# Optimization experiments

Hardware: AMD Instinct MI355X
Metric: run time of the kernel (lower is better)

Reference implementation:

```python
import jax, jax.numpy as jnp
import numpy as np

V, H, I, L = 32000, 1024, 2048, 4
NH, NKV, HD = 16, 8, 64
E, K = 4, 2
B, S = 2, 1024
NEG = jnp.finfo(jnp.float32).min


def setup_inputs() -> dict:
    key = jax.random.key(0)
    ks = jax.random.split(key, 11)
    w = lambda k, shape: jax.random.normal(k, shape, jnp.float32) * 0.02
    return dict(
        input_ids=jax.random.randint(ks[0], (B, S), 0, V),
        embed=w(ks[1], (V, H)),
        Wq=w(ks[2], (L, H, NH * HD)),
        Wk=w(ks[3], (L, H, NKV * HD)),
        Wv=w(ks[4], (L, H, NKV * HD)),
        Wo=w(ks[5], (L, NH * HD, H)),
        ln1=jnp.ones((L, H), jnp.float32),
        ln2=jnp.ones((L, H), jnp.float32),
        gate=w(ks[6], (L, H, E)),
        Wg=w(ks[7], (L, E, H, I)),
        Wu=w(ks[8], (L, E, H, I)),
        Wd=w(ks[9], (L, E, I, H)),
        norm_w=jnp.ones((H,), jnp.float32),
        lm_head=w(ks[10], (H, V)),
    )


def rmsnorm(x, w, eps=1e-6):
    var = jnp.mean(x * x, axis=-1, keepdims=True)
    return w * (x * jax.lax.rsqrt(var + eps))


def forward(input_ids, embed, Wq, Wk, Wv, Wo, ln1, ln2, gate, Wg, Wu, Wd, norm_w, lm_head):
    b, s = input_ids.shape
    h = embed[input_ids]  # [B,S,H]
    mask = jnp.where(jnp.triu(jnp.ones((s, s), bool), 1), NEG, 0.0)[None, None]  # causal [1,1,S,S]
    inv_sqrt_hd = 1.0 / np.sqrt(HD)
    rep = NH // NKV

    def step(h, p):
        wq, wk, wv, wo, l1, l2, gw, wg, wu, wd = p
        x = rmsnorm(h, l1)
        q = (x @ wq).reshape(b, s, NH, HD).transpose(0, 2, 1, 3)    # [B,NH,S,HD]
        k = (x @ wk).reshape(b, s, NKV, HD).transpose(0, 2, 1, 3)   # [B,NKV,S,HD]
        v = (x @ wv).reshape(b, s, NKV, HD).transpose(0, 2, 1, 3)
        k = jnp.repeat(k, rep, axis=1)  # GQA repeat_kv
        v = jnp.repeat(v, rep, axis=1)
        scores = jnp.einsum('bhqd,bhkd->bhqk', q, k) * inv_sqrt_hd + mask
        attn = jax.nn.softmax(scores, axis=-1)
        o = jnp.einsum('bhqk,bhkd->bhqd', attn, v).transpose(0, 2, 1, 3).reshape(b, s, NH * HD)
        h = h + o @ wo
        # MoE FFN (top-k routing, combine via per-expert gate weights)
        x = rmsnorm(h, l2).reshape(b * s, H)              # [T,H]
        probs = jax.nn.softmax(x @ gw, axis=-1)           # [T,E]
        topk_p, topk_i = jax.lax.top_k(probs, K)          # [T,K]
        comb = jnp.sum(topk_p[..., None] * jax.nn.one_hot(topk_i, E, dtype=x.dtype), axis=1)  # [T,E]
        g = jax.nn.silu(jnp.einsum('th,ehi->eti', x, wg))  # [E,T,I]
        u = jnp.einsum('th,ehi->eti', x, wu)
        eo = jnp.einsum('eti,eih->eth', g * u, wd)         # [E,T,H]
        moe = jnp.einsum('eth,te->th', eo, comb).reshape(b, s, H)
        return h + moe, None

    h, _ = jax.lax.scan(step, h, (Wq, Wk, Wv, Wo, ln1, ln2, gate, Wg, Wu, Wd))
    return rmsnorm(h, norm_w) @ lm_head  # [B,S,V]


def reference(input_ids, embed, Wq, Wk, Wv, Wo, ln1, ln2, gate, Wg, Wu, Wd, norm_w, lm_head):
    return forward(input_ids, embed, Wq, Wk, Wv, Wo, ln1, ln2, gate, Wg, Wu, Wd, norm_w, lm_head)
```

## Files before the change

kernel.cpp:

```cpp
#include <hip/hip_runtime.h>

#define T_ 2048
#define H_ 1024
#define S_ 1024
#define V_ 32000
#define I_ 2048
#define NHD 1024
#define KVD 512

typedef unsigned short u16;
typedef unsigned int u32;
typedef __attribute__((ext_vector_type(8))) short s16x8;
typedef __attribute__((ext_vector_type(4))) float f32x4;

__device__ __forceinline__ u16 f2b(float f){ u32 x=__builtin_bit_cast(u32,f); return (u16)((x+0x7fffu+((x>>16)&1u))>>16); }
__device__ __forceinline__ float b2f(u16 u){ return __builtin_bit_cast(float,(u32)u<<16); }
__device__ __forceinline__ float wsum(float v){ for(int o=32;o;o>>=1) v+=__shfl_xor(v,o); return v; }

__device__ __forceinline__ void gl16(const void* g, void* l){
  __builtin_amdgcn_global_load_lds(
      (const __attribute__((address_space(1))) unsigned int*)g,
      (__attribute__((address_space(3))) unsigned int*)l, 16, 0, 0);
}

__global__ void k_embed(const int* __restrict__ ids, const float* __restrict__ emb,
                        float* __restrict__ h, int* __restrict__ cnt){
  if(blockIdx.x==0 && threadIdx.x<16) cnt[threadIdx.x]=0;
  int t = blockIdx.x;
  long src = (long)ids[t]*H_;
  ((float4*)(h + (long)t*H_))[threadIdx.x] = ((const float4*)(emb+src))[threadIdx.x];
}

__global__ void k_rms_sp(const float* __restrict__ h, const float* __restrict__ w,
                         u16* __restrict__ xhi, u16* __restrict__ xlo){
  int wid = threadIdx.x>>6, lane = threadIdx.x&63;
  int t = blockIdx.x*4 + wid;
  const float* row = h + (long)t*H_;
  float v[16]; float ss=0.f;
  #pragma unroll
  for(int j=0;j<16;j++){ v[j]=row[j*64+lane]; ss += v[j]*v[j]; }
  ss = wsum(ss);
  float rstd = rsqrtf(ss/(float)H_ + 1e-6f);
  #pragma unroll
  for(int j=0;j<16;j++){
    int idx=j*64+lane;
    float y = v[j]*rstd*w[idx];
    u16 hv = f2b(y);
    xhi[(long)t*H_+idx] = hv;
    if(xlo) xlo[(long)t*H_+idx] = f2b(y - b2f(hv));
  }
}

__global__ void k_router(const float* __restrict__ h, const float* __restrict__ lw,
                         const float* __restrict__ gate, float* __restrict__ comb,
                         int* __restrict__ lists, int* __restrict__ cnt, int2* __restrict__ epos,
                         u16* __restrict__ xhi, u16* __restrict__ xlo){
  int wid = threadIdx.x>>6, lane = threadIdx.x&63;
  int t = blockIdx.x*4+wid;
  const float* row = h + (long)t*H_;
  float v[16]; float ss=0.f;
  #pragma unroll
  for(int j=0;j<16;j++){ v[j]=row[j*64+lane]; ss+=v[j]*v[j]; }
  ss = wsum(ss);
  float rstd = rsqrtf(ss/(float)H_+1e-6f);
  float a0=0,a1=0,a2=0,a3=0;
  #pragma unroll
  for(int j=0;j<16;j++){
    int idx=j*64+lane;
    float y = v[j]*rstd*lw[idx];
    u16 hv = f2b(y);
    xhi[(long)t*H_+idx] = hv;
    xlo[(long)t*H_+idx] = f2b(y - b2f(hv));
    float4 g4 = ((const float4*)gate)[idx];
    a0 += y*g4.x; a1 += y*g4.y; a2 += y*g4.z; a3 += y*g4.w;
  }
  a0=wsum(a0); a1=wsum(a1); a2=wsum(a2); a3=wsum(a3);
  if(lane==0){
    float p[4]={a0,a1,a2,a3};
    float m = fmaxf(fmaxf(p[0],p[1]),fmaxf(p[2],p[3]));
    float s=0; for(int e=0;e<4;e++){ p[e]=__expf(p[e]-m); s+=p[e]; }
    for(int e=0;e<4;e++) p[e]/=s;
    int i1=0; for(int e=1;e<4;e++) if(p[e]>p[i1]) i1=e;
    int i2=-1; for(int e=0;e<4;e++){ if(e==i1) continue; if(i2<0||p[e]>p[i2]) i2=e; }
    float* c = comb + (long)t*4;
    for(int e=0;e<4;e++) c[e] = (e==i1||e==i2)? p[e] : 0.f;
    int p1 = atomicAdd(&cnt[i1],1); lists[i1*T_+p1]=t;
    int p2 = atomicAdd(&cnt[i2],1); lists[i2*T_+p2]=t;
    epos[t] = make_int2((p1<<2)|i1, (p2<<2)|i2);
  }
}

__global__ void k_transpose(const float* __restrict__ in, u16* __restrict__ hi, u16* __restrict__ lo,
                            int R, int C, long zi, long zo){
  __shared__ float tile[32][33];
  in += (long)blockIdx.z*zi; hi += (long)blockIdx.z*zo; if(lo) lo += (long)blockIdx.z*zo;
  int c0 = blockIdx.x*32, r0 = blockIdx.y*32;
  int tx = threadIdx.x, ty = threadIdx.y;
  #pragma unroll
  for(int i=0;i<4;i++) tile[ty+8*i][tx] = in[(long)(r0+ty+8*i)*C + c0+tx];
  __syncthreads();
  #pragma unroll
  for(int i=0;i<4;i++){
    int cc=ty+8*i; float v = tile[tx][cc];
    u16 hv = f2b(v);
    long idx = (long)(c0+cc)*R + r0+tx;
    hi[idx] = hv;
    if(lo) lo[idx] = f2b(v - b2f(hv));
  }
}

__global__ void k_wtrans(const float* __restrict__ Wq, const float* __restrict__ Wk,
                         const float* __restrict__ Wv, const float* __restrict__ Wo,
                         const float* __restrict__ Wg, const float* __restrict__ Wu,
                         const float* __restrict__ Wd,
                         u16* __restrict__ qkvh, u16* __restrict__ qkvl,
                         u16* __restrict__ oh, u16* __restrict__ ol,
                         u16* __restrict__ gh, u16* __restrict__ gl_,
                         u16* __restrict__ uh, u16* __restrict__ ul,
                         u16* __restrict__ dh, u16* __restrict__ dl)
{
  __shared__ float tile[32][33];
  int id = blockIdx.x;
  const float* in; u16 *hi, *lo; int R, C, bx, by;
  if(id < 1024){ in=Wq; hi=qkvh; lo=qkvl; R=1024; C=1024; bx=id&31; by=id>>5; }
  else if(id < 1536){ id-=1024; in=Wk; hi=qkvh+1048576; lo=qkvl+1048576; R=1024; C=512; bx=id&15; by=id>>4; }
  else if(id < 2048){ id-=1536; in=Wv; hi=qkvh+1572864; lo=qkvl+1572864; R=1024; C=512; bx=id&15; by=id>>4; }
  else if(id < 3072){ id-=2048; in=Wo; hi=oh; lo=ol; R=1024; C=1024; bx=id&31; by=id>>5; }
  else if(id < 11264){ id-=3072; int z=id>>11, r2=id&2047;
    in=Wg+(size_t)z*H_*I_; hi=gh+(size_t)z*I_*H_; lo=gl_+(size_t)z*I_*H_;
    R=1024; C=2048; bx=r2&63; by=r2>>6; }
  else if(id < 19456){ id-=11264; int z=id>>11, r2=id&2047;
    in=Wu+(size_t)z*H_*I_; hi=uh+(size_t)z*I_*H_; lo=ul+(size_t)z*I_*H_;
    R=1024; C=2048; bx=r2&63; by=r2>>6; }
  else { id-=19456; int z=id>>11, r2=id&2047;
    in=Wd+(size_t)z*I_*H_; hi=dh+(size_t)z*H_*I_; lo=dl+(size_t)z*H_*I_;
    R=2048; C=1024; bx=r2&31; by=r2>>5; }
  int c0=bx*32, r0=by*32, tx=threadIdx.x, ty=threadIdx.y;
  #pragma unroll
  for(int i=0;i<4;i++) tile[ty+8*i][tx] = in[(long)(r0+ty+8*i)*C + c0+tx];
  __syncthreads();
  #pragma unroll
  for(int i=0;i<4;i++){
    int cc=ty+8*i; float v = tile[tx][cc];
    u16 hv = f2b(v);
    long idx = (long)(c0+cc)*R + r0+tx;
    hi[idx] = hv;
    lo[idx] = f2b(v - b2f(hv));
  }
}

__global__ void k_combine(float* __restrict__ h, const float* __restrict__ eo,
                          const int2* __restrict__ epos, const float* __restrict__ comb,
                          const float* __restrict__ wn, u16* __restrict__ xhi, u16* __restrict__ xlo){
  int t = blockIdx.x, c = threadIdx.x;
  int lane = c&63, wid = c>>6;
  int2 ep = epos[t];
  int e1 = ep.x&3, p1 = ep.x>>2, e2 = ep.y&3, p2 = ep.y>>2;
  float c1 = comb[t*4+e1], c2 = comb[t*4+e2];
  float4 a = ((const float4*)(eo + (long)(e1*T_+p1)*H_))[c];
  float4 b = ((const float4*)(eo + (long)(e2*T_+p2)*H_))[c];
  float4* hp = (float4*)(h + (long)t*H_) + c;
  float4 hv = *hp;
  hv.x += c1*a.x + c2*b.x; hv.y += c1*a.y + c2*b.y;
  hv.z += c1*a.z + c2*b.z; hv.w += c1*a.w + c2*b.w;
  *hp = hv;
  __shared__ float red[4];
  float ss = hv.x*hv.x + hv.y*hv.y + hv.z*hv.z + hv.w*hv.w;
  ss = wsum(ss);
  if(lane==0) red[wid]=ss;
  __syncthreads();
  float tot = red[0]+red[1]+red[2]+red[3];
  float rstd = rsqrtf(tot*(1.f/1024.f) + 1e-6f);
  float4 wv = ((const float4*)wn)[c];
  float y0=hv.x*rstd*wv.x, y1=hv.y*rstd*wv.y, y2=hv.z*rstd*wv.z, y3=hv.w*rstd*wv.w;
  ushort4 Hv; Hv.x=f2b(y0); Hv.y=f2b(y1); Hv.z=f2b(y2); Hv.w=f2b(y3);
  ((ushort4*)(xhi + (long)t*H_))[c] = Hv;
  if(xlo){
    ushort4 Lv;
    Lv.x=f2b(y0-b2f(Hv.x)); Lv.y=f2b(y1-b2f(Hv.y));
    Lv.z=f2b(y2-b2f(Hv.z)); Lv.w=f2b(y3-b2f(Hv.w));
    ((ushort4*)(xlo + (long)t*H_))[c] = Lv;
  }
}

__global__ __launch_bounds__(512) void k_flash(
  const u16* __restrict__ qh_g, const u16* __restrict__ ql_g,
  const u16* __restrict__ kh_g, const u16* __restrict__ kl_g,
  const u16* __restrict__ vth_g, const u16* __restrict__ vtl_g,
  u16* __restrict__ oh_g, u16* __restrict__ ol_g)
{
  __shared__ alignas(16) u16 Kh[8192], Kl[8192];
  __shared__ alignas(16) u16 Vh[8192], Vl[8192];
  __shared__ alignas(16) u16 Ph[16384], Pl[16384];
  const int qt = blockIdx.x, hh = blockIdx.y, b = blockIdx.z;
  const int hk = hh>>1;
  const int lane = threadIdx.x&63, w = threadIdx.x>>6;
  const int rA = lane&15, kg = (lane>>4)*8;

  s16x8 qfh[2], qfl[2];
  {
    long t = (long)(b*1024+qt*128) + w*16 + rA;
    const u16* qp = qh_g + t*NHD + hh*64;
    const u16* qp2= ql_g + t*NHD + hh*64;
    qfh[0]=*(const s16x8*)(qp + kg);      qfh[1]=*(const s16x8*)(qp + 32 + kg);
    qfl[0]=*(const s16x8*)(qp2 + kg);     qfl[1]=*(const s16x8*)(qp2 + 32 + kg);
  }

  const int ktend = qt+1;
  {
    const u16* kp = kh_g + ((long)(b*1024))*KVD + hk*64;
    const u16* kp2= kl_g + ((long)(b*1024))*KVD + hk*64;
    #pragma unroll
    for(int s=0;s<2;s++){
      int idx=s*8+w, hf=idx>>3, g=idx&7;
      int row = g*16 + (lane>>2);
      int c8  = hf*32 + (lane&3)*8;
      gl16(kp  + (long)row*KVD + c8, &Kh[hf*4096 + g*512]);
      gl16(kp2 + (long)row*KVD + c8, &Kl[hf*4096 + g*512]);
    }
  }

  f32x4 Oa[4];
  float mrun[4], lrun[4];
  #pragma unroll
  for(int jn=0;jn<4;jn++){ f32x4 zv={0.f,0.f,0.f,0.f}; Oa[jn]=zv; }
  #pragma unroll
  for(int r=0;r<4;r++){ mrun[r]=-3.0e38f; lrun[r]=0.f; }

  __syncthreads();

  for(int kt=0; kt<ktend; kt++){
    {
      const u16* vp = vth_g + (long)b*((long)KVD*S_) + (long)(hk*64)*S_ + kt*128;
      const u16* vp2= vtl_g + (long)b*((long)KVD*S_) + (long)(hk*64)*S_ + kt*128;
      #pragma unroll
      for(int s=0;s<2;s++){
        int idx=s*8+w, ks=idx>>2, g=idx&3;
        int dr = g*16 + (lane>>2);
        int k8 = (lane&3)*8;
        gl16(vp  + (long)dr*S_ + ks*32 + k8, &Vh[ks*2048 + g*512]);
        gl16(vp2 + (long)dr*S_ + ks*32 + k8, &Vl[ks*2048 + g*512]);
      }
    }

    f32x4 Sf[8];
    #pragma unroll
    for(int j=0;j<8;j++){ f32x4 zv={0.f,0.f,0.f,0.f}; Sf[j]=zv; }
    #pragma unroll
    for(int k2=0;k2<2;k2++){
      s16x8 bh[8],bl[8];
      #pragma unroll
      for(int j=0;j<8;j++){
        int ky = j*16+rA;
        bh[j]=*(const s16x8*)&Kh[k2*4096 + ky*32 + kg];
        bl[j]=*(const s16x8*)&Kl[k2*4096 + ky*32 + kg];
      }
      #pragma unroll
      for(int j=0;j<8;j++){
        Sf[j]=__builtin_amdgcn_mfma_f32_16x16x32_bf16(qfh[k2],bh[j],Sf[j],0,0,0);
        Sf[j]=__builtin_amdgcn_mfma_f32_16x16x32_bf16(qfh[k2],bl[j],Sf[j],0,0,0);
        Sf[j]=__builtin_amdgcn_mfma_f32_16x16x32_bf16(qfl[k2],bh[j],Sf[j],0,0,0);
      }
    }

    const bool last = (kt==ktend-1);
    #pragma unroll
    for(int j=0;j<8;j++)
      #pragma unroll
      for(int r=0;r<4;r++){
        float sv = Sf[j][r]*0.125f;
        if(last){
          int qr = qt*128 + w*16 + ((lane>>4)<<2) + r;
          int ky = kt*128 + j*16 + (lane&15);
          if(ky>qr) sv = -3.0e38f;
        }
        Sf[j][r]=sv;
      }

    float mt[4];
    #pragma unroll
    for(int r=0;r<4;r++){
      float v = Sf[0][r];
      #pragma unroll
      for(int j=1;j<8;j++) v = fmaxf(v, Sf[j][r]);
      v=fmaxf(v,__shfl_xor(v,1)); v=fmaxf(v,__shfl_xor(v,2));
      v=fmaxf(v,__shfl_xor(v,4)); v=fmaxf(v,__shfl_xor(v,8));
      mt[r]=v;
    }

    #pragma unroll
    for(int r=0;r<4;r++){
      float mo=mrun[r];
      float mn=fmaxf(mo,mt[r]);
      float al_=__expf(mo-mn);
      mrun[r]=mn;
      lrun[r]*=al_;
      #pragma unroll
      for(int jn=0;jn<4;jn++) Oa[jn][r]*=al_;
    }

    float ls[4];
    #pragma unroll
    for(int r=0;r<4;r++) ls[r]=0.f;
    #pragma unroll
    for(int j=0;j<8;j++)
      #pragma unroll
      for(int r=0;r<4;r++){
        int q  = w*16+((lane>>4)<<2)+r;
        int ky = j*16+(lane&15);
        float pv=__expf(Sf[j][r]-mrun[r]);
        ls[r]+=pv;
        u16 hv=f2b(pv);
        int a=(ky>>5)*4096 + q*32 + (ky&31);
        Ph[a]=hv; Pl[a]=f2b(pv-b2f(hv));
      }
    #pragma unroll
    for(int r=0;r<4;r++){
      float v=ls[r];
      v+=__shfl_xor(v,1); v+=__shfl_xor(v,2); v+=__shfl_xor(v,4); v+=__shfl_xor(v,8);
      lrun[r]+=v;
    }
    __syncthreads();

    if(kt+1<ktend){
      const u16* kp = kh_g + ((long)(b*1024+(kt+1)*128))*KVD + hk*64;
      const u16* kp2= kl_g + ((long)(b*1024+(kt+1)*128))*KVD + hk*64;
      #pragma unroll
      for(int s=0;s<2;s++){
        int idx=s*8+w, hf=idx>>3, g=idx&7;
        int row = g*16 + (lane>>2);
        int c8  = hf*32 + (lane&3)*8;
        gl16(kp  + (long)row*KVD + c8, &Kh[hf*4096 + g*512]);
        gl16(kp2 + (long)row*KVD + c8, &Kl[hf*4096 + g*512]);
      }
    }

    #pragma unroll
    for(int ks=0;ks<4;ks++){
      s16x8 pah,pal,vbh[4],vbl[4];
      int q = w*16+rA;
      pah=*(const s16x8*)&Ph[ks*4096 + q*32 + kg];
      pal=*(const s16x8*)&Pl[ks*4096 + q*32 + kg];
      #pragma unroll
      for(int jn=0;jn<4;jn++){
        int d = jn*16+rA;
        vbh[jn]=*(const s16x8*)&Vh[ks*2048 + d*32 + kg];
        vbl[jn]=*(const s16x8*)&Vl[ks*2048 + d*32 + kg];
      }
      #pragma unroll
      for(int jn=0;jn<4;jn++){
        Oa[jn]=__builtin_amdgcn_mfma_f32_16x16x32_bf16(pah,vbh[jn],Oa[jn],0,0,0);
        Oa[jn]=__builtin_amdgcn_mfma_f32_16x16x32_bf16(pah,vbl[jn],Oa[jn],0,0,0);
        Oa[jn]=__builtin_amdgcn_mfma_f32_16x16x32_bf16(pal,vbh[jn],Oa[jn],0,0,0);
      }
    }
    __syncthreads();
  }

  #pragma unroll
  for(int jn=0;jn<4;jn++)
    #pragma unroll
    for(int r=0;r<4;r++){
      long t = (long)b*1024 + qt*128 + w*16+((lane>>4)<<2)+r;
      int col = hh*64 + jn*16 + (lane&15);
      float ov = Oa[jn][r] / lrun[r];
      u16 hv=f2b(ov);
      oh_g[t*NHD+col]=hv;
      ol_g[t*NHD+col]=f2b(ov-b2f(hv));
    }
}

__global__ __launch_bounds__(256) void k_qkv(
  const u16* __restrict__ xhi, const u16* __restrict__ xlo,
  const u16* __restrict__ Bh, const u16* __restrict__ Bl,
  u16* __restrict__ qhi, u16* __restrict__ qlo,
  u16* __restrict__ khi, u16* __restrict__ klo,
  u16* __restrict__ vthi, u16* __restrict__ vtlo)
{
  __shared__ alignas(16) u16 As[2*128*64], Bs[2*128*64];
  const int m0=blockIdx.x*128, n0=blockIdx.y*128;
  const int tid=threadIdx.x, lane=tid&63, w=tid>>6, wr=w>>1, wc=w&1;
  const int rsub = lane>>3;
  const int col8 = ((lane&7) ^ (rsub&7))*8;
  const int kq = lane>>4;
  f32x4 acc[4][4];
  #pragma unroll
  for(int i=0;i<4;i++)
    #pragma unroll
    for(int j=0;j<4;j++){ f32x4 zv={0.f,0.f,0.f,0.f}; acc[i][j]=zv; }

  for(int kt=0;kt<16;kt++){
    const int k0=kt*64;
    __syncthreads();
    #pragma unroll
    for(int s=0;s<4;s++){
      int ch=s*4+w; int row=ch*8+rsub;
      gl16(xhi + (long)(m0+row)*H_ + k0+col8, &As[ch*512]);
      gl16(xlo + (long)(m0+row)*H_ + k0+col8, &As[8192+ch*512]);
      gl16(Bh  + (long)(n0+row)*H_ + k0+col8, &Bs[ch*512]);
      gl16(Bl  + (long)(n0+row)*H_ + k0+col8, &Bs[8192+ch*512]);
    }
    __syncthreads();
    #pragma unroll
    for(int ks=0;ks<2;ks++){
      s16x8 ah[4],al[4],bh[4],bl[4];
      #pragma unroll
      for(int i=0;i<4;i++){
        int row = wr*64+i*16+(lane&15);
        int sl = ((ks*4+kq) ^ (row&7))*8;
        ah[i]=*(const s16x8*)&As[row*64+sl];
        al[i]=*(const s16x8*)&As[8192+row*64+sl];
      }
      #pragma unroll
      for(int j=0;j<4;j++){
        int row = wc*64+j*16+(lane&15);
        int sl = ((ks*4+kq) ^ (row&7))*8;
        bh[j]=*(const s16x8*)&Bs[row*64+sl];
        bl[j]=*(const s16x8*)&Bs[8192+row*64+sl];
      }
      #pragma unroll
      for(int i=0;i<4;i++)
        #pragma unroll
        for(int j=0;j<4;j++){
          acc[i][j]=__builtin_amdgcn_mfma_f32_16x16x32_bf16(ah[i],bh[j],acc[i][j],0,0,0);
          acc[i][j]=__builtin_amdgcn_mfma_f32_16x16x32_bf16(ah[i],bl[j],acc[i][j],0,0,0);
          acc[i][j]=__builtin_amdgcn_mfma_f32_16x16x32_bf16(al[i],bh[j],acc[i][j],0,0,0);
        }
    }
  }

  #pragma unroll
  for(int i=0;i<4;i++){
    #pragma unroll
    for(int j=0;j<4;j++){
      const int gm0 = m0 + wr*64 + i*16 + ((lane>>4)<<2);
      const int gn  = n0 + wc*64 + j*16 + (lane&15);
      #pragma unroll
      for(int r=0;r<4;r++){
        const int gm = gm0+r;
        float v = acc[i][j][r];
        u16 hv = f2b(v);
        u16 lv = f2b(v - b2f(hv));
        if(gn < 1024){
          long idx=(long)gm*NHD+gn; qhi[idx]=hv; qlo[idx]=lv;
        } else if(gn < 1536){
          long idx=(long)gm*KVD+(gn-1024); khi[idx]=hv; klo[idx]=lv;
        } else {
          long idx=((long)(gm>>10)<<19) + (long)(gn-1536)*S_ + (gm&1023);
          vthi[idx]=hv; vtlo[idx]=lv;
        }
      }
    }
  }
}

__global__ __launch_bounds__(256) void k_moe_ug(
  const u16* __restrict__ xhi, const u16* __restrict__ xlo,
  const u16* __restrict__ Wuh, const u16* __restrict__ Wul,
  const u16* __restrict__ Wgh, const u16* __restrict__ Wgl,
  u16* __restrict__ guh, u16* __restrict__ gul,
  const int* __restrict__ lists, const int* __restrict__ cntp)
{
  const int bb = blockIdx.x;
  const int xcd = bb&7, bidx = bb>>3;
  const int grp = xcd + 8*(bidx>>4);
  const int mslot = bidx&15;
  const int e = grp>>5;
  const int n0 = (grp&31)*64;
  const int m0 = mslot*128;
  const int ce = cntp[e];
  if(m0>=ce) return;
  const int* ridx = lists + e*T_;
  const u16* Buh_g = Wuh + (size_t)e*H_*I_;
  const u16* Bul_g = Wul + (size_t)e*H_*I_;
  const u16* Bgh_g = Wgh + (size_t)e*H_*I_;
  const u16* Bgl_g = Wgl + (size_t)e*H_*I_;
  __shared__ alignas(16) u16 Ah[128*64], Al[128*64];
  __shared__ alignas(16) u16 Buh[64*64], Bul[64*64], Bgh[64*64], Bgl[64*64];
  const int tid=threadIdx.x, lane=tid&63, w=tid>>6;
  const int wr=w>>1, wc=w&1;
  const int rsub = lane>>3;
  const int col8 = ((lane&7) ^ (rsub&7))*8;
  const int kq = lane>>4;
  int arA[4];
  #pragma unroll
  for(int s=0;s<4;s++){ int idx=m0 + (s*4+w)*8 + rsub; arA[s]=ridx[idx<ce?idx:ce-1]; }
  f32x4 au[4][2], ag[4][2];
  #pragma unroll
  for(int i=0;i<4;i++)
    #pragma unroll
    for(int j=0;j<2;j++){ f32x4 zv={0.f,0.f,0.f,0.f}; au[i][j]=zv; ag[i][j]=zv; }

  for(int kt=0;kt<16;kt++){
    const int k0=kt*64;
    __syncthreads();
    #pragma unroll
    for(int s=0;s<4;s++){
      int ch=s*4+w;
      gl16(xhi + (long)arA[s]*H_ + k0+col8, &Ah[ch*512]);
      gl16(xlo + (long)arA[s]*H_ + k0+col8, &Al[ch*512]);
    }
    #pragma unroll
    for(int s=0;s<2;s++){
      int ch=s*4+w;
      int brow = n0 + ch*8 + rsub;
      gl16(Buh_g + (long)brow*H_ + k0+col8, &Buh[ch*512]);
      gl16(Bul_g + (long)brow*H_ + k0+col8, &Bul[ch*512]);
      gl16(Bgh_g + (long)brow*H_ + k0+col8, &Bgh[ch*512]);
      gl16(Bgl_g + (long)brow*H_ + k0+col8, &Bgl[ch*512]);
    }
    __syncthreads();
    #pragma unroll
    for(int ks=0;ks<2;ks++){
      s16x8 fah[4],fal[4],fbuh[2],fbul[2],fbgh[2],fbgl[2];
      #pragma unroll
      for(int i=0;i<4;i++){
        int row = wr*64+i*16+(lane&15);
        int sl = ((ks*4+kq) ^ (row&7))*8;
        fah[i]=*(const s16x8*)&Ah[row*64+sl];
        fal[i]=*(const s16x8*)&Al[row*64+sl];
      }
      #pragma unroll
      for(int j=0;j<2;j++){
        int row = wc*32+j*16+(lane&15);
        int sl = ((ks*4+kq) ^ (row&7))*8;
        fbuh[j]=*(const s16x8*)&Buh[row*64+sl];
        fbul[j]=*(const s16x8*)&Bul[row*64+sl];
        fbgh[j]=*(const s16x8*)&Bgh[row*64+sl];
        fbgl[j]=*(const s16x8*)&Bgl[row*64+sl];
      }
      #pragma unroll
      for(int i=0;i<4;i++)
        #pragma unroll
        for(int j=0;j<2;j++){
          au[i][j]=__builtin_amdgcn_mfma_f32_16x16x32_bf16(fah[i],fbuh[j],au[i][j],0,0,0);
          au[i][j]=__builtin_amdgcn_mfma_f32_16x16x32_bf16(fah[i],fbul[j],au[i][j],0,0,0);
          au[i][j]=__builtin_amdgcn_mfma_f32_16x16x32_bf16(fal[i],fbuh[j],au[i][j],0,0,0);
          ag[i][j]=__builtin_amdgcn_mfma_f32_16x16x32_bf16(fah[i],fbgh[j],ag[i][j],0,0,0);
          ag[i][j]=__builtin_amdgcn_mfma_f32_16x16x32_bf16(fah[i],fbgl[j],ag[i][j],0,0,0);
          ag[i][j]=__builtin_amdgcn_mfma_f32_16x16x32_bf16(fal[i],fbgh[j],ag[i][j],0,0,0);
        }
    }
  }

  #pragma unroll
  for(int i=0;i<4;i++){
    #pragma unroll
    for(int j=0;j<2;j++){
      const int gm0 = m0 + wr*64 + i*16 + ((lane>>4)<<2);
      const int gn  = n0 + wc*32 + j*16 + (lane&15);
      #pragma unroll
      for(int r=0;r<4;r++){
        const int gm = gm0+r;
        if(gm<ce){
          float uu=au[i][j][r], gg=ag[i][j][r];
          float val = (gg/(1.f+__expf(-gg)))*uu;
          long idx = (long)(e*T_+gm)*I_ + gn;
          u16 hv=f2b(val);
          guh[idx]=hv; gul[idx]=f2b(val-b2f(hv));
        }
      }
    }
  }
}

template<int BM,int BN,int WM,int WN,int BKT,bool SPL,int EPI,int GATH,bool SWZ,bool PIPE>
__launch_bounds__(WM*WN*64)
__global__ void k_gemm(const u16* __restrict__ Ahip, const u16* __restrict__ Alop,
                       const u16* __restrict__ Bhip, const u16* __restrict__ Blop,
                       void* __restrict__ Cp, void* __restrict__ auxp,
                       const int* __restrict__ cntp,
                       int Kdim, int lda, int ldb, int ldc,
                       long zA, long zB, int zBdiv, long zC,
                       float scale)
{
  constexpr int NT = WM*WN*64;
  constexpr int Wv = NT/64;
  constexpr int WMT = BM/WM, WNT = BN/WN;
  constexpr int MF = WMT/16, NF = WNT/16;
  constexpr int LPR = BKT/8;
  constexpr int LR  = 64/LPR;
  constexpr int ACn = (BM/LR)/Wv;
  constexpr int BCn = (BN/LR)/Wv;
  constexpr int KS  = BKT/32;
  constexpr int ABY = (SPL?2:1)*BM*BKT*2;
  constexpr int BBY = (SPL?2:1)*BN*BKT*2;
  constexpr int STEP = ABY+BBY;
  constexpr int SBY = (PIPE?2:1)*STEP;
  constexpr int CBY = (EPI==8) ? WM*16*(BN+4)*4 : 0;
  constexpr int SMB = SBY > CBY ? SBY : CBY;
  static_assert(ACn>=1 && BCn>=1, "chunks");
  __shared__ alignas(16) char smem[SMB];
  float* Csf = (float*)smem;
  constexpr int SL = T_/BM;
  int m0, n0, eid_ = 0, cnt = 0;
  if constexpr (GATH==4){
    constexpr int NTN = H_/BN;
    const int bb = blockIdx.x;
    const int xcd = bb&7, bidx = bb>>3;
    const int grp = xcd + 8*(bidx/SL);
    const int mslot = bidx%SL;
    eid_ = grp/NTN; n0 = (grp%NTN)*BN; m0 = mslot*BM;
    cnt = cntp[eid_]; if(m0>=cnt) return;
  } else if constexpr (SWZ){
    int nx = gridDim.x;
    int l = blockIdx.y*nx + blockIdx.x;
    int q = (nx*gridDim.y)>>3;
    int wid = (l&7)*q + (l>>3);
    m0 = (wid % nx)*BM; n0 = (wid / nx)*BN;
  } else {
    m0 = blockIdx.x*BM; n0 = blockIdx.y*BN;
  }
  const int z = blockIdx.z;
  const int tid = threadIdx.x, lane = tid&63, w = tid>>6;
  const int wr = w/WN, wc = w%WN;
  const int rsub = lane/LPR;
  const int col8 = (((lane%LPR) ^ (rsub&(LPR-1))))*8;
  const int kq = lane>>4;
  const u16* Ahi = Ahip + (long)z*zA + (GATH==4 ? (long)eid_*T_*lda : 0);
  const u16* Alo = SPL ? (Alop + (long)z*zA + (GATH==4 ? (long)eid_*T_*lda : 0)) : (const u16*)nullptr;
  const u16* Bh  = Bhip + (long)(z/zBdiv)*zB + (GATH==4 ? (long)eid_*zB : 0);
  const u16* Bl  = SPL ? (Blop + (long)(z/zBdiv)*zB + (GATH==4 ? (long)eid_*zB : 0)) : (const u16*)nullptr;

  f32x4 acc[MF][NF];
  #pragma unroll
  for(int i=0;i<MF;i++)
    #pragma unroll
    for(int j=0;j<NF;j++){ f32x4 zv={0.f,0.f,0.f,0.f}; acc[i][j]=zv; }

  const int ktend = Kdim/BKT;

  auto stage = [&](int kt, int bo){
    u16* As = (u16*)(smem + bo);
    u16* Bs = (u16*)(smem + bo + ABY);
    const int k0 = kt*BKT;
    #pragma unroll
    for(int s=0;s<ACn;s++){
      int ch = s*Wv + w;
      int arow = m0 + ch*LR + rsub;
      if constexpr (GATH==4){ arow = arow < cnt ? arow : cnt-1; }
      gl16(Ahi + (long)arow*lda + k0+col8, &As[ch*512]);
      if constexpr (SPL) gl16(Alo + (long)arow*lda + k0+col8, &As[BM*BKT + ch*512]);
    }
    #pragma unroll
    for(int s=0;s<BCn;s++){
      int ch = s*Wv + w;
      int brow = n0 + ch*LR + rsub;
      gl16(Bh + (long)brow*ldb + k0+col8, &Bs[ch*512]);
      if constexpr (SPL) gl16(Bl + (long)brow*ldb + k0+col8, &Bs[BN*BKT + ch*512]);
    }
  };

  auto compute = [&](int bo){
    u16* As = (u16*)(smem + bo);
    u16* Bs = (u16*)(smem + bo + ABY);
    #pragma unroll
    for(int ks=0;ks<KS;ks++){
      s16x8 ah[MF], al[MF], bh[NF], bl[NF];
      #pragma unroll
      for(int i=0;i<MF;i++){
        int row = wr*WMT+i*16+(lane&15);
        int sl = ((ks*4+kq) ^ (row&(LPR-1)))*8;
        ah[i]=*(const s16x8*)&As[row*BKT+sl];
        if constexpr (SPL) al[i]=*(const s16x8*)&As[BM*BKT+row*BKT+sl];
      }
      #pragma unroll
      for(int j=0;j<NF;j++){
        int row = wc*WNT+j*16+(lane&15);
        int sl = ((ks*4+kq) ^ (row&(LPR-1)))*8;
        bh[j]=*(const s16x8*)&Bs[row*BKT+sl];
        if constexpr (SPL) bl[j]=*(const s16x8*)&Bs[BN*BKT+row*BKT+sl];
      }
      #pragma unroll
      for(int i=0;i<MF;i++)
        #pragma unroll
        for(int j=0;j<NF;j++){
          acc[i][j]=__builtin_amdgcn_mfma_f32_16x16x32_bf16(ah[i],bh[j],acc[i][j],0,0,0);
          if constexpr (SPL){
            acc[i][j]=__builtin_amdgcn_mfma_f32_16x16x32_bf16(ah[i],bl[j],acc[i][j],0,0,0);
            acc[i][j]=__builtin_amdgcn_mfma_f32_16x16x32_bf16(al[i],bh[j],acc[i][j],0,0,0);
          }
        }
    }
  };

  if constexpr (PIPE){
    stage(0, 0);
    __syncthreads();
    for(int kt=0;kt<ktend;kt++){
      int cur = kt&1;
      if(kt+1<ktend) stage(kt+1, (cur^1)*STEP);
      compute(cur*STEP);
      __syncthreads();
    }
  } else {
    for(int kt=0;kt<ktend;kt++){
      __syncthreads();
      stage(kt, 0);
      __syncthreads();
      compute(0);
    }
  }

  if constexpr (EPI==8){
    float* C = (float*)Cp + (long)z*zC;
    #pragma unroll
    for(int i=0;i<MF;i++){
      __syncthreads();
      #pragma unroll
      for(int j=0;j<NF;j++)
        #pragma unroll
        for(int r=0;r<4;r++)
          Csf[wr*16*(BN+4) + (((lane>>4)<<2)+r)*(BN+4) + wc*WNT + j*16 + (lane&15)] = acc[i][j][r]*scale;
      __syncthreads();
      const int rrow = tid>>3;
      const int wri = rrow>>4, r16 = rrow&15;
      const long gm = m0 + wri*WMT + i*16 + r16;
      #pragma unroll
      for(int s=0;s<BN/32;s++){
        int c0 = ((tid&7) + s*8)*4;
        const float* Cr = &Csf[wri*16*(BN+4) + r16*(BN+4)];
        float4 vv = { Cr[c0], Cr[c0+1], Cr[c0+2], Cr[c0+3] };
        *(float4*)(C + gm*ldc + n0 + c0) = vv;
      }
    }
    return;
  }

  #pragma unroll
  for(int i=0;i<MF;i++){
    #pragma unroll
    for(int j=0;j<NF;j++){
      const int gm0 = m0 + wr*WMT + i*16 + ((lane>>4)<<2);
      const int gn  = n0 + wc*WNT + j*16 + (lane&15);
      #pragma unroll
      for(int r=0;r<4;r++){
        const int gm = gm0+r;
        const float v = acc[i][j][r];
        const bool live = (GATH==0) || (gm < cnt);
        if constexpr (EPI==1){
          if(live) ((float*)Cp + (long)z*zC)[(long)gm*ldc+gn] = v*scale;
        } else if constexpr (EPI==2){
          float* C = (float*)Cp; C[(long)gm*ldc+gn] += v;
        } else if constexpr (EPI==7){
          if(live) ((float*)Cp)[(long)(eid_*T_+gm)*ldc+gn] = v*scale;
        } else if constexpr (EPI==9){
          u16* Ch = (u16*)Cp + (long)z*zC;
          u16* Cl = (u16*)auxp + (long)z*zC;
          long idx = (long)gm*ldc+gn;
          u16 hv = f2b(v);
          Ch[idx]=hv; Cl[idx]=f2b(v-b2f(hv));
        }
      }
    }
  }
}

extern "C" void kernel_launch(void* const* d_in, const int* in_sizes, int n_in,
                              void* d_out, int out_size, void* d_ws, size_t ws_size,
                              hipStream_t stream)
{
  (void)in_sizes; (void)n_in; (void)out_size;
  const int*   ids   = (const int*)d_in[0];
  const float* emb   = (const float*)d_in[1];
  const float* Wq    = (const float*)d_in[2];
  const float* Wk    = (const float*)d_in[3];
  const float* Wv    = (const float*)d_in[4];
  const float* Wo    = (const float*)d_in[5];
  const float* ln1   = (const float*)d_in[6];
  const float* ln2   = (const float*)d_in[7];
  const float* gate  = (const float*)d_in[8];
  const float* Wg    = (const float*)d_in[9];
  const float* Wu    = (const float*)d_in[10];
  const float* Wd    = (const float*)d_in[11];
  const float* normw = (const float*)d_in[12];
  const float* lmh   = (const float*)d_in[13];

  char* p = (char*)d_ws;
  auto carve = [&](size_t bytes)->void*{ void* r=p; p += (bytes+255)&~(size_t)255; return r; };
  float* h    = (float*)carve((size_t)T_*H_*4);
  u16*   xhi  = (u16*)  carve((size_t)T_*H_*2);
  u16*   xlo  = (u16*)  carve((size_t)T_*H_*2);
  u16*   qhi  = (u16*)  carve((size_t)T_*NHD*2);
  u16*   qlo  = (u16*)  carve((size_t)T_*NHD*2);
  u16*   khi  = (u16*)  carve((size_t)T_*KVD*2);
  u16*   klo  = (u16*)  carve((size_t)T_*KVD*2);
  u16*   vthi = (u16*)  carve((size_t)T_*KVD*2);
  u16*   vtlo = (u16*)  carve((size_t)T_*KVD*2);
  u16*   ohi  = (u16*)  carve((size_t)T_*NHD*2);
  u16*   olo  = (u16*)  carve((size_t)T_*NHD*2);
  float* comb = (float*)carve((size_t)T_*4*4);
  int*   cnt  = (int*)  carve((size_t)16*4);
  int*   lists= (int*)  carve((size_t)4*T_*4);
  int2*  epos = (int2*) carve((size_t)T_*8);
  char*  U    = (char*) carve((size_t)112*1024*1024);
  u16*   wp   = (u16*)  carve((size_t)56623104*2);
  if ((size_t)(p - (char*)d_ws) > ws_size) return;

  u16*   guh  = (u16*)U;
  u16*   gul  = (u16*)(U + 33554432);
  float* eo   = (float*)(U + 67108864);

  u16 *WqkvTh = wp,          *WqkvTl = wp+2097152;
  u16 *WoTh = wp+4194304,    *WoTl = wp+5242880;
  u16 *WgTh = wp+6291456,    *WgTl = wp+14680064;
  u16 *WuTh = wp+23068672,   *WuTl = wp+31457280;
  u16 *WdTh = wp+39845888,   *WdTl = wp+48234496;

  dim3 tb(32,8);

  k_embed<<<T_,256,0,stream>>>(ids, emb, h, cnt);

  for(int l=0;l<4;l++){
    k_wtrans<<<27648,tb,0,stream>>>(
      Wq+(size_t)l*H_*NHD, Wk+(size_t)l*H_*KVD, Wv+(size_t)l*H_*KVD, Wo+(size_t)l*NHD*H_,
      Wg+(size_t)l*4*H_*I_, Wu+(size_t)l*4*H_*I_, Wd+(size_t)l*4*I_*H_,
      WqkvTh, WqkvTl, WoTh, WoTl, WgTh, WgTl, WuTh, WuTl, WdTh, WdTl);

    if(l==0) k_rms_sp<<<T_/4,256,0,stream>>>(h, ln1, xhi, xlo);

    k_qkv<<<dim3(16,16),256,0,stream>>>(xhi, xlo, WqkvTh, WqkvTl, qhi, qlo, khi, klo, vthi, vtlo);

    k_flash<<<dim3(8,16,2),512,0,stream>>>(qhi, qlo, khi, klo, vthi, vtlo, ohi, olo);

    k_gemm<64,128,2,2,64,true,2,0,false,false><<<dim3(32,8,1),256,0,stream>>>(
      ohi, olo, WoTh, WoTl, h, nullptr, nullptr, NHD, NHD, NHD, H_, 0,0,1,0, 0.f);

    k_router<<<T_/4,256,0,stream>>>(h, ln2+(size_t)l*H_, gate+(size_t)l*H_*4, comb, lists, cnt+l*4, epos, xhi, xlo);

    k_moe_ug<<<2048,256,0,stream>>>(xhi, xlo, WuTh, WuTl, WgTh, WgTl, guh, gul, lists, cnt+l*4);
    k_gemm<128,128,2,2,64,true,7,4,false,false><<<512,256,0,stream>>>(
      guh, gul, WdTh, WdTl, eo, nullptr, cnt+l*4, I_, I_, I_, H_, 0, (long)I_*H_, 1, 0, 1.f);
    if(l<3)
      k_combine<<<T_,256,0,stream>>>(h, eo, epos, comb, ln1+(size_t)(l+1)*H_, xhi, xlo);
    else
      k_combine<<<T_,256,0,stream>>>(h, eo, epos, comb, normw, xhi, nullptr);
  }

  k_transpose<<<dim3(1000,32),tb,0,stream>>>(lmh, wp, nullptr, H_, V_, 0,0);
  k_gemm<128,128,2,2,64,false,8,0,true,true><<<dim3(16,250,1),256,0,stream>>>(
    xhi, nullptr, wp, nullptr, (float*)d_out, nullptr, nullptr, H_, H_, H_, V_, 0,0,1,0, 1.f);
}
```

Before: 1.858 ms.

## Add dedicated 256x256-tile LM-head GEMM kernel with swizzled LDS double buffering

Replaces the generic 128x128 GEMM used for the final LM-head projection with a specialized kernel. It uses 256x256 output tiles over 512 threads, XOR-swizzled LDS, global-to-LDS async double buffering with explicit waitcnt, and a block-index remap that groups tiles for L2 reuse. The output is staged through LDS so it can be written as coalesced float4 stores. The larger tiles cut the operand traffic per output, at the cost of heavy register and LDS use (128KB shared) and lower occupancy.

```diff
diff --git a/kernel.cpp b/kernel.cpp
--- a/kernel.cpp
+++ b/kernel.cpp
@@ -560,6 +560,104 @@
           guh[idx]=hv; gul[idx]=f2b(val-b2f(hv));
         }
       }
+    }
+  }
+}
+
+__global__ __launch_bounds__(512) void k_lmhead(
+  const u16* __restrict__ A, const u16* __restrict__ B, float* __restrict__ C)
+{
+  __shared__ alignas(16) u16 smem[65536];
+  const int bb = blockIdx.x;
+  const int wid = (bb&7)*125 + (bb>>3);
+  const int m0 = (wid&7)*256;
+  const int n0 = (wid>>3)*256;
+  const int tid = threadIdx.x, lane = tid&63, w = tid>>6;
+  const int wr = w>>2, wc = w&3;
+  const int rsub = lane>>3;
+  const int col8 = ((lane&7) ^ rsub)*8;
+  const int kq = lane>>4;
+
+  f32x4 acc[8][4];
+  #pragma unroll
+  for(int i=0;i<8;i++)
+    #pragma unroll
+    for(int j=0;j<4;j++){ f32x4 zv={0.f,0.f,0.f,0.f}; acc[i][j]=zv; }
+
+  auto stage4 = [&](int kt, int c){
+    const int k0 = kt*64;
+    #pragma unroll
+    for(int q=0;q<4;q++){
+      const u16* src = (q<2) ? A : B;
+      u16* dst = &smem[(q<2 ? 0 : 32768) + c*16384 + (q&1)*8192];
+      const long row0 = ((q<2) ? m0 : n0) + (q&1)*128;
+      #pragma unroll
+      for(int s=0;s<2;s++){
+        int ch = s*8 + w;
+        long row = row0 + ch*8 + rsub;
+        gl16(src + row*H_ + k0 + col8, dst + ch*512);
+      }
+    }
+  };
+
+  stage4(0, 0);
+
+  for(int kt=0;kt<16;kt++){
+    const int c = kt&1;
+    __builtin_amdgcn_s_barrier();
+    __builtin_amdgcn_sched_barrier(0);
+    if(kt<15) stage4(kt+1, c^1);
+    __builtin_amdgcn_sched_barrier(0);
+    if(kt<15) asm volatile("s_waitcnt vmcnt(8)" ::: "memory");
+    else      asm volatile("s_waitcnt vmcnt(0)" ::: "memory");
+    __builtin_amdgcn_sched_barrier(0);
+    __builtin_amdgcn_s_barrier();
+    __builtin_amdgcn_sched_barrier(0);
+    #pragma unroll
+    for(int p=0;p<4;p++){
+      const int ks = p>>1, ih = p&1;
+      s16x8 af[4], bf[4];
+      #pragma unroll
+      for(int ii=0;ii<4;ii++){
+        int row = wr*128 + (ih*4+ii)*16 + (lane&15);
+        int sl = ((ks*4+kq) ^ (row&7))*8;
+        af[ii] = *(const s16x8*)&smem[c*16384 + row*64 + sl];
+      }
+      #pragma unroll
+      for(int j=0;j<4;j++){
+        int row = wc*64 + j*16 + (lane&15);
+        int sl = ((ks*4+kq) ^ (row&7))*8;
+        bf[j] = *(const s16x8*)&smem[32768 + c*16384 + row*64 + sl];
+      }
+      __builtin_amdgcn_s_setprio(1);
+      #pragma unroll
+      for(int ii=0;ii<4;ii++)
+        #pragma unroll
+        for(int j=0;j<4;j++)
+          acc[ih*4+ii][j] = __builtin_amdgcn_mfma_f32_16x16x32_bf16(af[ii], bf[j], acc[ih*4+ii][j], 0,0,0);
+      __builtin_amdgcn_s_setprio(0);
+    }
+  }
+
+  float* Csf = (float*)smem;
+  #pragma unroll
+  for(int i=0;i<8;i++){
+    __syncthreads();
+    #pragma unroll
+    for(int j=0;j<4;j++)
+      #pragma unroll
+      for(int r=0;r<4;r++)
+        Csf[wr*4160 + (((lane>>4)<<2)+r)*260 + wc*64 + j*16 + (lane&15)] = acc[i][j][r];
+    __syncthreads();
+    const int rrow = tid>>4;
+    const int wri = rrow>>4, r16 = rrow&15;
+    const long gm = m0 + wri*128 + i*16 + r16;
+    #pragma unroll
+    for(int s=0;s<4;s++){
+      int c0 = ((tid&15) + s*16)*4;
+      const float* Cr = &Csf[wri*4160 + r16*260];
+      float4 vv = { Cr[c0], Cr[c0+1], Cr[c0+2], Cr[c0+3] };
+      *(float4*)(C + gm*(long)V_ + n0 + c0) = vv;
     }
   }
 }
@@ -838,6 +936,5 @@
   }
 
   k_transpose<<<dim3(1000,32),tb,0,stream>>>(lmh, wp, nullptr, H_, V_, 0,0);
-  k_gemm<128,128,2,2,64,false,8,0,true,true><<<dim3(16,250,1),256,0,stream>>>(
-    xhi, nullptr, wp, nullptr, (float*)d_out, nullptr, nullptr, H_, H_, H_, V_, 0,0,1,0, 1.f);
-}
+  k_lmhead<<<1000,512,0,stream>>>(xhi, wp, (float*)d_out);
+}
```

New measurement: 1.828 ms. No clear change (-1.6%).
